# Kernel tuning notes

Measured on AMD Instinct MI355X. Metric: run time of the kernel, lower is better.

## Reference

```python
import jax, jax.numpy as jnp
import numpy as np

B, S, D, H, DK, DV, L = 2, 2048, 256, 8, 32, 32, 3


def positional_encoding(seq_len, d_model):
    pos = jnp.arange(seq_len, dtype=jnp.float32)[:, None]
    div = jnp.exp(jnp.arange(0, d_model, 2, dtype=jnp.float32) * (-np.log(10000.0) / d_model))
    pe = jnp.zeros((seq_len, d_model), jnp.float32)
    pe = pe.at[:, 0::2].set(jnp.sin(pos * div))
    pe = pe.at[:, 1::2].set(jnp.cos(pos * div))
    return pe  # [S, D]


def setup_inputs() -> dict:
    key = jax.random.key(0)
    ks = jax.random.split(key, 5)
    w_scale = 1.0 / np.sqrt(D)
    return {
        "seq_inputs": jax.random.normal(ks[0], (B, S, D), dtype=jnp.float32),
        "Wq": jax.random.normal(ks[1], (L, D, H * DK), dtype=jnp.float32) * w_scale,
        "Wk": jax.random.normal(ks[2], (L, D, H * DK), dtype=jnp.float32) * w_scale,
        "Wv": jax.random.normal(ks[3], (L, D, H * DV), dtype=jnp.float32) * w_scale,
        "Wfc": jax.random.normal(ks[4], (L, H * DV, D), dtype=jnp.float32) * w_scale,
    }


def reference(seq_inputs, Wq, Wk, Wv, Wfc):
    # positional encoding add (dropout is identity in eval)
    x = seq_inputs + positional_encoding(S, D)[None]  # [B,S,D]
    inv_sqrt_dk = 1.0 / np.sqrt(DK)

    def layer(x, w):
        wq, wk, wv, wfc = w
        q = (x @ wq).reshape(B, S, H, DK).transpose(0, 2, 1, 3)  # [B,H,S,DK]
        k = (x @ wk).reshape(B, S, H, DK).transpose(0, 2, 1, 3)
        v = (x @ wv).reshape(B, S, H, DV).transpose(0, 2, 1, 3)
        scores = jnp.einsum('bhqd,bhkd->bhqk', q, k) * inv_sqrt_dk  # [B,H,S,S]
        attn = jax.nn.softmax(scores, axis=-1)
        ctx = jnp.einsum('bhqk,bhkd->bhqd', attn, v)  # [B,H,S,DV]
        ctx = ctx.transpose(0, 2, 1, 3).reshape(B, S, H * DV)
        # NOTE: original torch code has NO residual add and NO layernorm applied
        return ctx @ wfc, attn

    out, attns = jax.lax.scan(layer, x, (Wq, Wk, Wv, Wfc))
    return out, attns  # out: [B,S,D], attns: [L,B,H,S,S]
```

## Files before the change

kernel.cpp:

```cpp
#include <hip/hip_runtime.h>
#include <hip/hip_bf16.h>

#define BB 2
#define SS 2048
#define DD 256
#define HH 8
#define DKK 32
#define DVV 32
#define LL 3

typedef __hip_bfloat16 bf16;
typedef __attribute__((ext_vector_type(8))) short bfrag;
typedef __attribute__((ext_vector_type(4))) float f4;

__device__ __forceinline__ bfrag ld8(const bf16* p) {
  return *reinterpret_cast<const bfrag*>(p);
}

__global__ __launch_bounds__(256) void cast_weights_k(const float* __restrict__ wq,
                                                      const float* __restrict__ wk,
                                                      const float* __restrict__ wv,
                                                      const float* __restrict__ wfc,
                                                      bf16* __restrict__ wts) {
  int e = blockIdx.x * 256 + threadIdx.x;
  int mat = e >> 16;
  int t = mat & 3;
  int l = mat >> 2;
  int kk = (e >> 8) & 255;
  int n = e & 255;
  const float* src = (t == 0) ? wq : (t == 1) ? wk : (t == 2) ? wv : wfc;
  float v = src[((size_t)l * 256 + kk) * 256 + n];
  wts[(size_t)mat * 65536 + (size_t)n * 256 + kk] = __float2bfloat16(v);
}

__global__ __launch_bounds__(256) void pe_add_k(const float* __restrict__ seq,
                                                bf16* __restrict__ xbf) {
  int e = blockIdx.x * 256 + threadIdx.x;
  int d = e & 255;
  int m = e >> 8;
  int s = m & (SS - 1);
  int i2 = d >> 1;
  float div = __expf((float)(2 * i2) * (-9.210340371976184f / 256.0f));
  float ang = (float)s * div;
  float pe = (d & 1) ? __cosf(ang) : __sinf(ang);
  xbf[e] = __float2bfloat16(seq[e] + pe);
}

__global__ __launch_bounds__(256) void proj_k(const bf16* __restrict__ xbf,
                                              const bf16* __restrict__ wl,
                                              bf16* __restrict__ q,
                                              bf16* __restrict__ k,
                                              bf16* __restrict__ vt) {
  int lane = threadIdx.x & 63;
  int wv = threadIdx.x >> 6;
  int c = lane & 15, g = lane >> 4;
  int t = blockIdx.y >> 2;
  int n0 = (blockIdx.y & 3) * 64;
  int m0 = blockIdx.x * 64 + wv * 16;
  const bf16* wt = wl + (size_t)t * 65536;
  const bf16* arow = xbf + (size_t)(m0 + c) * 256 + g * 8;
  f4 acc[4];
#pragma unroll
  for (int i = 0; i < 4; ++i) acc[i] = (f4){0.f, 0.f, 0.f, 0.f};
#pragma unroll
  for (int kk = 0; kk < 8; ++kk) {
    bfrag af = ld8(arow + kk * 32);
#pragma unroll
    for (int ns = 0; ns < 4; ++ns) {
      bfrag bfr = ld8(wt + (size_t)(n0 + ns * 16 + c) * 256 + kk * 32 + g * 8);
      acc[ns] = __builtin_amdgcn_mfma_f32_16x16x32_bf16(af, bfr, acc[ns], 0, 0, 0);
    }
  }
#pragma unroll
  for (int ns = 0; ns < 4; ++ns) {
#pragma unroll
    for (int r = 0; r < 4; ++r) {
      int m = m0 + g * 4 + r;
      int n = n0 + ns * 16 + c;
      int b = m >> 11, s = m & (SS - 1);
      int h = n >> 5, d = n & 31;
      bf16 v = __float2bfloat16(acc[ns][r]);
      if (t == 0)      q[((size_t)(b * HH + h) * SS + s) * DKK + d] = v;
      else if (t == 1) k[((size_t)(b * HH + h) * SS + s) * DKK + d] = v;
      else             vt[((size_t)(b * HH + h) * DVV + d) * SS + s] = v;
    }
  }
}

__global__ __launch_bounds__(256) void fc_k(const bf16* __restrict__ ctxbf,
                                            const bf16* __restrict__ wt,
                                            bf16* __restrict__ xbf,
                                            float* __restrict__ fout, int wf) {
  int lane = threadIdx.x & 63;
  int wv = threadIdx.x >> 6;
  int c = lane & 15, g = lane >> 4;
  int n0 = blockIdx.y * 64;
  int m0 = blockIdx.x * 64 + wv * 16;
  const bf16* arow = ctxbf + (size_t)(m0 + c) * 256 + g * 8;
  f4 acc[4];
#pragma unroll
  for (int i = 0; i < 4; ++i) acc[i] = (f4){0.f, 0.f, 0.f, 0.f};
#pragma unroll
  for (int kk = 0; kk < 8; ++kk) {
    bfrag af = ld8(arow + kk * 32);
#pragma unroll
    for (int ns = 0; ns < 4; ++ns) {
      bfrag bfr = ld8(wt + (size_t)(n0 + ns * 16 + c) * 256 + kk * 32 + g * 8);
      acc[ns] = __builtin_amdgcn_mfma_f32_16x16x32_bf16(af, bfr, acc[ns], 0, 0, 0);
    }
  }
#pragma unroll
  for (int ns = 0; ns < 4; ++ns) {
#pragma unroll
    for (int r = 0; r < 4; ++r) {
      int m = m0 + g * 4 + r;
      int n = n0 + ns * 16 + c;
      float v = acc[ns][r];
      xbf[(size_t)m * 256 + n] = __float2bfloat16(v);
      if (wf) fout[(size_t)m * 256 + n] = v;
    }
  }
}

__global__ __launch_bounds__(256) void attn_light_k(const bf16* __restrict__ q,
                                                    const bf16* __restrict__ k,
                                                    const bf16* __restrict__ vt,
                                                    float* __restrict__ inv_out,
                                                    bf16* __restrict__ ctxbf) {
  const float C2 = 0.2550350812540738f;
  int lane = threadIdx.x & 63;
  int wv = threadIdx.x >> 6;
  int c = lane & 15, g = lane >> 4;
  int bh = blockIdx.y;
  int b = bh >> 3, h = bh & 7;
  int s0 = blockIdx.x * 64 + wv * 16;
  const bf16* qb = q + ((size_t)bh * SS + s0) * DKK;
  const bf16* kb = k + (size_t)bh * SS * DKK;
  const bf16* vb = vt + (size_t)bh * DVV * SS;
  bfrag qf = ld8(qb + c * DKK + g * 8);
  const f4 z = {0.f, 0.f, 0.f, 0.f};

  __shared__ __align__(16) bf16 pbf[4][16][40];
  float sums[4] = {0.f, 0.f, 0.f, 0.f};
  f4 acc0 = z, acc1 = z;
  for (int kc2 = 0; kc2 < SS / 32; ++kc2) {
#pragma unroll
    for (int t = 0; t < 2; ++t) {
      bfrag kf = ld8(kb + (size_t)(kc2 * 32 + t * 16 + c) * DKK + g * 8);
      f4 sc = __builtin_amdgcn_mfma_f32_16x16x32_bf16(qf, kf, z, 0, 0, 0);
#pragma unroll
      for (int r = 0; r < 4; ++r) {
        float e = __builtin_amdgcn_exp2f(sc[r] * C2);
        sums[r] += e;
        pbf[wv][g * 4 + r][t * 16 + c] = __float2bfloat16(e);
      }
    }
    bfrag pa = ld8(&pbf[wv][c][g * 8]);
    bfrag vf0 = ld8(vb + (size_t)c * SS + kc2 * 32 + g * 8);
    acc0 = __builtin_amdgcn_mfma_f32_16x16x32_bf16(pa, vf0, acc0, 0, 0, 0);
    bfrag vf1 = ld8(vb + (size_t)(16 + c) * SS + kc2 * 32 + g * 8);
    acc1 = __builtin_amdgcn_mfma_f32_16x16x32_bf16(pa, vf1, acc1, 0, 0, 0);
  }
#pragma unroll
  for (int mm = 1; mm < 16; mm <<= 1) {
#pragma unroll
    for (int r = 0; r < 4; ++r) sums[r] += __shfl_xor(sums[r], mm, 64);
  }
#pragma unroll
  for (int r = 0; r < 4; ++r) {
    float iv = 1.0f / sums[r];
    if (c == 0) inv_out[(size_t)bh * SS + s0 + g * 4 + r] = iv;
    int srow = s0 + g * 4 + r;
    size_t base = ((size_t)b * SS + srow) * 256 + h * 32;
    ctxbf[base + c] = __float2bfloat16(acc0[r] * iv);
    ctxbf[base + 16 + c] = __float2bfloat16(acc1[r] * iv);
  }
}

__global__ __launch_bounds__(256, 4) void attn_store_k(const bf16* __restrict__ qs,
                                                       const bf16* __restrict__ ks,
                                                       const float* __restrict__ inv,
                                                       float* __restrict__ aout) {
  const float C2 = 0.2550350812540738f;
  int lane = threadIdx.x & 63;
  int wv = threadIdx.x >> 6;
  int c = lane & 15, g = lane >> 4;
  int lbh = blockIdx.z * BB * HH + blockIdx.y;
  int s0 = blockIdx.x * 64 + wv * 16;
  const bf16* qb = qs + ((size_t)lbh * SS + s0) * DKK;
  const bf16* kb = ks + (size_t)lbh * SS * DKK;
  bfrag qf = ld8(qb + c * DKK + g * 8);
  f4 invr = *reinterpret_cast<const f4*>(inv + (size_t)lbh * SS + s0 + g * 4);
  const f4 z = {0.f, 0.f, 0.f, 0.f};

  __shared__ __align__(16) float pf[4][16 * 64];
  float* pw = pf[wv];
  float* arow = aout + ((size_t)lbh * SS + s0) * SS;

  for (int kc4 = 0; kc4 < SS / 64; ++kc4) {
#pragma unroll
    for (int t = 0; t < 4; ++t) {
      bfrag kf = ld8(kb + (size_t)(kc4 * 64 + t * 16 + c) * DKK + g * 8);
      f4 sc = __builtin_amdgcn_mfma_f32_16x16x32_bf16(qf, kf, z, 0, 0, 0);
#pragma unroll
      for (int r = 0; r < 4; ++r) {
        float p = __builtin_amdgcn_exp2f(sc[r] * C2) * invr[r];
        int row = g * 4 + r;
        int col = t * 16 + c;
        pw[row * 64 + (((col >> 2) ^ row) << 2) + (col & 3)] = p;
      }
    }
#pragma unroll
    for (int qq = 0; qq < 4; ++qq) {
      int row = qq * 4 + g;
      int col4 = c;
      f4 v = *reinterpret_cast<f4*>(&pw[row * 64 + ((col4 ^ row) << 2)]);
      *reinterpret_cast<f4*>(&arow[(size_t)row * SS + kc4 * 64 + (col4 << 2)]) = v;
    }
  }
}

extern "C" void kernel_launch(void* const* d_in, const int* in_sizes, int n_in,
                              void* d_out, int out_size, void* d_ws, size_t ws_size,
                              hipStream_t stream) {
  (void)in_sizes; (void)n_in; (void)out_size; (void)ws_size;
  const float* seq = (const float*)d_in[0];
  const float* Wq  = (const float*)d_in[1];
  const float* Wk  = (const float*)d_in[2];
  const float* Wv  = (const float*)d_in[3];
  const float* Wfc = (const float*)d_in[4];
  float* out = (float*)d_out;
  float* attns = out + (size_t)BB * SS * DD;

  const size_t MB2 = 2097152;
  char* ws = (char*)d_ws;
  bf16* wts  = (bf16*)(ws);
  bf16* xbf  = (bf16*)(ws + 1572864);
  bf16* vtb  = (bf16*)(ws + 1572864 + MB2);
  bf16* ctxb = (bf16*)(ws + 1572864 + 2 * MB2);
  bf16* qs   = (bf16*)(ws + 1572864 + 3 * MB2);
  bf16* ks   = (bf16*)(ws + 1572864 + 6 * MB2);
  float* invb = (float*)(ws + 1572864 + 9 * MB2);

  cast_weights_k<<<3072, 256, 0, stream>>>(Wq, Wk, Wv, Wfc, wts);
  pe_add_k<<<4096, 256, 0, stream>>>(seq, xbf);

  for (int l = 0; l < LL; ++l) {
    bf16* ql = qs + (size_t)l * BB * HH * SS * DKK;
    bf16* kl = ks + (size_t)l * BB * HH * SS * DKK;
    float* invl = invb + (size_t)l * BB * HH * SS;
    proj_k<<<dim3(64, 12), 256, 0, stream>>>(xbf, wts + (size_t)l * 4 * 65536, ql, kl, vtb);
    attn_light_k<<<dim3(SS / 64, BB * HH), 256, 0, stream>>>(ql, kl, vtb, invl, ctxb);
    fc_k<<<dim3(64, 4), 256, 0, stream>>>(ctxb, wts + ((size_t)l * 4 + 3) * 65536,
                                          xbf, out, (l == LL - 1) ? 1 : 0);
  }
  attn_store_k<<<dim3(SS / 64, BB * HH, LL), 256, 0, stream>>>(qs, ks, invb, attns);
}
```

Baseline: 389.5 us.

## Split attention key range across waves with shared-memory reduction

```diff
diff --git a/kernel.cpp b/kernel.cpp
--- a/kernel.cpp
+++ b/kernel.cpp
@@ -122,28 +122,31 @@
   }
 }
 
-__global__ __launch_bounds__(256) void attn_light_k(const bf16* __restrict__ q,
-                                                    const bf16* __restrict__ k,
-                                                    const bf16* __restrict__ vt,
-                                                    float* __restrict__ inv_out,
-                                                    bf16* __restrict__ ctxbf) {
+__global__ __launch_bounds__(256, 4) void attn_light_k(const bf16* __restrict__ q,
+                                                       const bf16* __restrict__ k,
+                                                       const bf16* __restrict__ vt,
+                                                       float* __restrict__ inv_out,
+                                                       bf16* __restrict__ ctxbf) {
   const float C2 = 0.2550350812540738f;
   int lane = threadIdx.x & 63;
   int wv = threadIdx.x >> 6;
   int c = lane & 15, g = lane >> 4;
   int bh = blockIdx.y;
   int b = bh >> 3, h = bh & 7;
-  int s0 = blockIdx.x * 64 + wv * 16;
+  int s0 = blockIdx.x * 16;
   const bf16* qb = q + ((size_t)bh * SS + s0) * DKK;
-  const bf16* kb = k + (size_t)bh * SS * DKK;
-  const bf16* vb = vt + (size_t)bh * DVV * SS;
+  const bf16* kb = k + ((size_t)bh * SS + wv * 512) * DKK;
+  const bf16* vb = vt + (size_t)bh * DVV * SS + wv * 512;
   bfrag qf = ld8(qb + c * DKK + g * 8);
   const f4 z = {0.f, 0.f, 0.f, 0.f};
 
   __shared__ __align__(16) bf16 pbf[4][16][40];
+  __shared__ float redsum[4][16];
+  __shared__ float redacc[4][16][32];
+
   float sums[4] = {0.f, 0.f, 0.f, 0.f};
   f4 acc0 = z, acc1 = z;
-  for (int kc2 = 0; kc2 < SS / 32; ++kc2) {
+  for (int kc2 = 0; kc2 < 16; ++kc2) {
 #pragma unroll
     for (int t = 0; t < 2; ++t) {
       bfrag kf = ld8(kb + (size_t)(kc2 * 32 + t * 16 + c) * DKK + g * 8);
@@ -166,18 +169,30 @@
 #pragma unroll
     for (int r = 0; r < 4; ++r) sums[r] += __shfl_xor(sums[r], mm, 64);
   }
+  if (c == 0) {
+#pragma unroll
+    for (int r = 0; r < 4; ++r) redsum[wv][g * 4 + r] = sums[r];
+  }
 #pragma unroll
   for (int r = 0; r < 4; ++r) {
-    float iv = 1.0f / sums[r];
-    if (c == 0) inv_out[(size_t)bh * SS + s0 + g * 4 + r] = iv;
-    int srow = s0 + g * 4 + r;
-    size_t base = ((size_t)b * SS + srow) * 256 + h * 32;
-    ctxbf[base + c] = __float2bfloat16(acc0[r] * iv);
-    ctxbf[base + 16 + c] = __float2bfloat16(acc1[r] * iv);
-  }
-}
-
-__global__ __launch_bounds__(256, 4) void attn_store_k(const bf16* __restrict__ qs,
+    redacc[wv][g * 4 + r][c] = acc0[r];
+    redacc[wv][g * 4 + r][16 + c] = acc1[r];
+  }
+  __syncthreads();
+  int t = threadIdx.x;
+#pragma unroll
+  for (int e = 0; e < 2; ++e) {
+    int idx = t + e * 256;
+    int row = idx >> 5, d = idx & 31;
+    float s = redsum[0][row] + redsum[1][row] + redsum[2][row] + redsum[3][row];
+    float a = redacc[0][row][d] + redacc[1][row][d] + redacc[2][row][d] + redacc[3][row][d];
+    float iv = 1.0f / s;
+    ctxbf[((size_t)b * SS + s0 + row) * 256 + h * 32 + d] = __float2bfloat16(a * iv);
+    if (d == 0) inv_out[(size_t)bh * SS + s0 + row] = iv;
+  }
+}
+
+__global__ __launch_bounds__(256, 6) void attn_store_k(const bf16* __restrict__ qs,
                                                        const bf16* __restrict__ ks,
                                                        const float* __restrict__ inv,
                                                        float* __restrict__ aout) {
@@ -250,7 +265,7 @@
     bf16* kl = ks + (size_t)l * BB * HH * SS * DKK;
     float* invl = invb + (size_t)l * BB * HH * SS;
     proj_k<<<dim3(64, 12), 256, 0, stream>>>(xbf, wts + (size_t)l * 4 * 65536, ql, kl, vtb);
-    attn_light_k<<<dim3(SS / 64, BB * HH), 256, 0, stream>>>(ql, kl, vtb, invl, ctxb);
+    attn_light_k<<<dim3(SS / 16, BB * HH), 256, 0, stream>>>(ql, kl, vtb, invl, ctxb);
     fc_k<<<dim3(64, 4), 256, 0, stream>>>(ctxb, wts + ((size_t)l * 4 + 3) * 65536,
                                           xbf, out, (l == LL - 1) ? 1 : 0);
   }
```

Result: slower. 400.8 us (+2.9%).
